# Kernel optimization log

Measured on AMD Instinct MI355X. Metric: run time of the kernel, lower is better.

The kernel has to match this reference:

```python
import jax, jax.numpy as jnp
import numpy as np

K = 1024  # init kwarg k


def setup_inputs() -> dict:
    key = jax.random.key(0)
    k1, k2 = jax.random.split(key)
    B, N, F = 8, 50000, 256
    node_embs = jax.random.normal(k1, (B, N, F), dtype=jnp.float32)
    mask = jnp.zeros((B, N), dtype=jnp.float32)  # additive mask (0 = keep)
    stdv = 1.0 / np.sqrt(F)
    scorer = jax.random.uniform(k2, (F, 1), dtype=jnp.float32, minval=-stdv, maxval=stdv)
    return {"node_embs": node_embs, "mask": mask, "scorer": scorer}


def reference(node_embs, mask, scorer):
    # scores: [B, N] = node_embs @ scorer / ||scorer||, plus additive mask
    scores = jnp.einsum('bnf,f->bn', node_embs, scorer[:, 0]) / jnp.linalg.norm(scorer)
    scores = scores + mask
    # top-k over node dim
    vals, topk_idx = jax.lax.top_k(scores, K)  # [B, K]
    # gather selected node embeddings and scale by tanh of their scores
    gathered = jnp.take_along_axis(node_embs, topk_idx[:, :, None], axis=1)  # [B, K, F]
    gate = jnp.tanh(jnp.take_along_axis(scores, topk_idx, axis=1))  # [B, K]
    out = gathered * gate[:, :, None]
    return out.transpose(0, 2, 1)  # [B, F, K]
```

## Files before the change

kernel.cpp:

```cpp
#include <hip/hip_runtime.h>
#include <math.h>

#define BB 8
#define NN 50000
#define FF 256
#define KK 1024
#define CHUNK 400
#define NCHUNK 125
#define NIT (CHUNK / 16)
#define CAPA 4096
#define RBLK 16

__device__ __forceinline__ unsigned long long key64(double x) {
    unsigned long long u = (unsigned long long)__double_as_longlong(x);
    u ^= (u & 0x8000000000000000ull) ? 0xFFFFFFFFFFFFFFFFull : 0x8000000000000000ull;
    return u;
}
__device__ __forceinline__ double key_to_double(unsigned long long k) {
    unsigned long long u = (k & 0x8000000000000000ull) ? (k ^ 0x8000000000000000ull) : ~k;
    return __longlong_as_double((long long)u);
}

__global__ __launch_bounds__(1024) void zero_kernel(unsigned int* __restrict__ p, int n) {
    int i = blockIdx.x * 1024 + threadIdx.x;
    if (i < n) p[i] = 0u;
}

__global__ __launch_bounds__(256) void score_kernel(const float* __restrict__ emb,
                                                    const float* __restrict__ mask,
                                                    const float* __restrict__ scorer,
                                                    double* __restrict__ scores,
                                                    unsigned int* __restrict__ ghist) {
    const int b    = blockIdx.x / NCHUNK;
    const int c    = blockIdx.x % NCHUNK;
    const int n0   = c * CHUNK;
    const int lane = threadIdx.x & 63;
    const int wave = threadIdx.x >> 6;
    const int s    = lane & 15;
    const int g    = lane >> 4;
    const int r0   = wave * 4 + g;

    __shared__ unsigned int h[2048];
    __shared__ float smask[CHUNK];
    for (int i = threadIdx.x; i < 2048; i += 256) h[i] = 0u;
    for (int i = threadIdx.x; i < CHUNK; i += 256) smask[i] = mask[b * NN + n0 + i];
    __syncthreads();

    double scd[16];
    {
        float4 f0 = ((const float4*)scorer)[s];
        float4 f1 = ((const float4*)scorer)[s + 16];
        float4 f2 = ((const float4*)scorer)[s + 32];
        float4 f3 = ((const float4*)scorer)[s + 48];
        scd[0]  = f0.x; scd[1]  = f0.y; scd[2]  = f0.z; scd[3]  = f0.w;
        scd[4]  = f1.x; scd[5]  = f1.y; scd[6]  = f1.z; scd[7]  = f1.w;
        scd[8]  = f2.x; scd[9]  = f2.y; scd[10] = f2.z; scd[11] = f2.w;
        scd[12] = f3.x; scd[13] = f3.y; scd[14] = f3.z; scd[15] = f3.w;
    }
    double n2 = 0.0;
    #pragma unroll
    for (int e = 0; e < 16; ++e) n2 += scd[e] * scd[e];
    #pragma unroll
    for (int off = 8; off; off >>= 1) n2 += __shfl_xor(n2, off, 64);
    const double inv_norm = 1.0 / sqrt(n2);

    const float* base  = emb + ((long)b * NN + n0) * FF;
    double*      sbase = scores + (long)b * NN + n0;

    auto step = [&](int it, const float4* vv) {
        double d = 0.0;
        #pragma unroll
        for (int i2 = 0; i2 < 4; ++i2) {
            d += (double)vv[i2].x * scd[4 * i2 + 0] + (double)vv[i2].y * scd[4 * i2 + 1] +
                 (double)vv[i2].z * scd[4 * i2 + 2] + (double)vv[i2].w * scd[4 * i2 + 3];
        }
        #pragma unroll
        for (int off = 8; off; off >>= 1) d += __shfl_xor(d, off, 64);
        if (s == 0) {
            const int row = it * 16 + r0;
            double sv = d * inv_norm + (double)smask[row];
            sbase[row] = sv;
            atomicAdd(&h[(unsigned)(key64(sv) >> 53)], 1u);
        }
    };

    const float* rp = base + r0 * FF;
    float4 v[4], w[4];
    #pragma unroll
    for (int i = 0; i < 4; ++i) v[i] = ((const float4*)rp)[s + 16 * i];

    for (int it = 0; it < NIT - 1; ++it) {
        rp += 16 * FF;
        #pragma unroll
        for (int i = 0; i < 4; ++i) w[i] = ((const float4*)rp)[s + 16 * i];
        step(it, v);
        #pragma unroll
        for (int i = 0; i < 4; ++i) v[i] = w[i];
    }
    step(NIT - 1, v);

    __syncthreads();
    unsigned int* gh = ghist + b * 2048;
    for (int i = threadIdx.x; i < 2048; i += 256) {
        unsigned int vv = h[i];
        if (vv) atomicAdd(&gh[i], vv);
    }
}

__global__ __launch_bounds__(1024) void candidates_kernel(const double* __restrict__ scores,
                                                          const unsigned int* __restrict__ ghist,
                                                          unsigned long long* __restrict__ ckey,
                                                          int* __restrict__ cidx,
                                                          unsigned int* __restrict__ ccnt) {
    const int b   = blockIdx.x;
    const int tid = threadIdx.x;
    const double* sc = scores + (long)b * NN;

    __shared__ unsigned int h[2048];
    __shared__ unsigned long long keyA[CAPA];
    __shared__ int idxA[CAPA];
    __shared__ int bin1_s, need2_s, bin2_s;
    __shared__ unsigned int cnt;

    const int i0 = tid, i1 = tid + 1024;

    h[i0] = ghist[b * 2048 + i0];
    h[i1] = ghist[b * 2048 + i1];
    if (tid == 0) cnt = 0u;
    __syncthreads();

    for (int off = 1; off < 2048; off <<= 1) {
        unsigned a0 = (i0 + off < 2048) ? h[i0 + off] : 0u;
        unsigned a1 = (i1 + off < 2048) ? h[i1 + off] : 0u;
        __syncthreads();
        h[i0] += a0; h[i1] += a1;
        __syncthreads();
    }
    if (h[i0] >= (unsigned)KK && (i0 == 2047 || h[i0 + 1] < (unsigned)KK)) {
        bin1_s = i0; need2_s = KK - (int)((i0 == 2047) ? 0u : h[i0 + 1]);
    }
    if (h[i1] >= (unsigned)KK && (i1 == 2047 || h[i1 + 1] < (unsigned)KK)) {
        bin1_s = i1; need2_s = KK - (int)((i1 == 2047) ? 0u : h[i1 + 1]);
    }
    __syncthreads();
    const unsigned long long bin1 = (unsigned long long)bin1_s;
    const unsigned need2 = (unsigned)need2_s;

    h[i0] = 0u; h[i1] = 0u;
    __syncthreads();
    for (int i = tid; i < NN / 2; i += 1024) {
        double2 v = ((const double2*)sc)[i];
        unsigned long long k0 = key64(v.x), k1 = key64(v.y);
        if ((k0 >> 53) == bin1) atomicAdd(&h[(unsigned)((k0 >> 42) & 2047ull)], 1u);
        if ((k1 >> 53) == bin1) atomicAdd(&h[(unsigned)((k1 >> 42) & 2047ull)], 1u);
    }
    __syncthreads();

    for (int off = 1; off < 2048; off <<= 1) {
        unsigned a0 = (i0 + off < 2048) ? h[i0 + off] : 0u;
        unsigned a1 = (i1 + off < 2048) ? h[i1 + off] : 0u;
        __syncthreads();
        h[i0] += a0; h[i1] += a1;
        __syncthreads();
    }
    if (h[i0] >= need2 && (i0 == 2047 || h[i0 + 1] < need2)) bin2_s = i0;
    if (h[i1] >= need2 && (i1 == 2047 || h[i1 + 1] < need2)) bin2_s = i1;
    __syncthreads();
    const unsigned long long pfx = (bin1 << 11) | (unsigned long long)bin2_s;

    for (int i = tid; i < NN / 2; i += 1024) {
        double2 v = ((const double2*)sc)[i];
        unsigned long long k0 = key64(v.x), k1 = key64(v.y);
        if ((k0 >> 42) >= pfx) {
            unsigned p = atomicAdd(&cnt, 1u);
            if (p < (unsigned)CAPA) { keyA[p] = k0; idxA[p] = 2 * i; }
        }
        if ((k1 >> 42) >= pfx) {
            unsigned p = atomicAdd(&cnt, 1u);
            if (p < (unsigned)CAPA) { keyA[p] = k1; idxA[p] = 2 * i + 1; }
        }
    }
    __syncthreads();
    const int M = (int)(cnt < (unsigned)CAPA ? cnt : (unsigned)CAPA);

    if (tid == 0) ccnt[b] = (unsigned)M;
    for (int i = tid; i < M; i += 1024) {
        ckey[b * CAPA + i] = keyA[i];
        cidx[b * CAPA + i] = idxA[i];
    }
}

__global__ __launch_bounds__(256) void rank_kernel(const unsigned long long* __restrict__ ckey,
                                                   const int* __restrict__ cidx,
                                                   const unsigned int* __restrict__ ccnt,
                                                   int* __restrict__ topk_idx,
                                                   float* __restrict__ gate) {
    const int b  = blockIdx.x >> 4;
    const int sl = blockIdx.x & (RBLK - 1);
    const int M  = (int)ccnt[b];
    const int r0 = sl * 256;
    if (r0 >= M) return;

    __shared__ unsigned long long k_s[CAPA];
    __shared__ int i_s[CAPA];

    const unsigned long long* kb = ckey + b * CAPA;
    const int* ib = cidx + b * CAPA;
    for (int i = threadIdx.x; i < M; i += 256) { k_s[i] = kb[i]; i_s[i] = ib[i]; }
    __syncthreads();

    const int r = r0 + threadIdx.x;
    if (r < M) {
        const unsigned long long kr = k_s[r];
        const int ir = i_s[r];
        int rank = 0;
        for (int j = 0; j < M; ++j) {
            const unsigned long long kj = k_s[j];
            rank += (kj > kr) || (kj == kr && i_s[j] < ir);
        }
        if (rank < KK) {
            topk_idx[b * KK + rank] = ir;
            gate[b * KK + rank]     = tanhf((float)key_to_double(kr));
        }
    }
}

__global__ __launch_bounds__(256) void gather_kernel(const float* __restrict__ emb,
                                                     const int* __restrict__ topk_idx,
                                                     const float* __restrict__ gate,
                                                     float* __restrict__ out) {
    const int b  = blockIdx.x >> 5;
    const int kt = blockIdx.x & 31;
    const int k0 = kt * 32;
    const int tid = threadIdx.x;

    __shared__ float tile[32][FF + 4];
    __shared__ int   s_idx[32];
    __shared__ float s_gate[32];

    if (tid < 32) {
        s_idx[tid]  = topk_idx[b * KK + k0 + tid];
        s_gate[tid] = gate[b * KK + k0 + tid];
    }
    __syncthreads();

    const int g = tid >> 6, lane = tid & 63;
    #pragma unroll
    for (int i = 0; i < 8; i++) {
        int kl = i * 4 + g;
        int row = s_idx[kl];
        float gt = s_gate[kl];
        float4 v = ((const float4*)(emb + ((long)b * NN + row) * FF))[lane];
        float* t = &tile[kl][lane * 4];
        t[0] = v.x * gt; t[1] = v.y * gt; t[2] = v.z * gt; t[3] = v.w * gt;
    }
    __syncthreads();

    const long outbase = ((long)b * FF) * KK + k0;
    #pragma unroll
    for (int c = 0; c < 32; c++) {
        int linear = c * 256 + tid;
        int f = linear >> 5;
        int k = linear & 31;
        out[outbase + (long)f * KK + k] = tile[k][f];
    }
}

extern "C" void kernel_launch(void* const* d_in, const int* in_sizes, int n_in,
                              void* d_out, int out_size, void* d_ws, size_t ws_size,
                              hipStream_t stream) {
    const float* emb    = (const float*)d_in[0];
    const float* mask   = (const float*)d_in[1];
    const float* scorer = (const float*)d_in[2];
    float* out = (float*)d_out;

    char* wsb = (char*)d_ws;
    double*             scores  = (double*)wsb;
    unsigned int*       ghist   = (unsigned int*)(wsb + sizeof(double) * BB * NN);
    int*                topkidx = (int*)((char*)ghist + sizeof(unsigned int) * BB * 2048);
    float*              gatep   = (float*)((char*)topkidx + sizeof(int) * BB * KK);
    unsigned long long* ckey    = (unsigned long long*)((char*)gatep + sizeof(float) * BB * KK);
    int*                cidx    = (int*)((char*)ckey + sizeof(unsigned long long) * BB * CAPA);
    unsigned int*       ccnt    = (unsigned int*)((char*)cidx + sizeof(int) * BB * CAPA);

    zero_kernel<<<16, 1024, 0, stream>>>(ghist, BB * 2048);
    score_kernel<<<BB * NCHUNK, 256, 0, stream>>>(emb, mask, scorer, scores, ghist);
    candidates_kernel<<<BB, 1024, 0, stream>>>(scores, ghist, ckey, cidx, ccnt);
    rank_kernel<<<BB * RBLK, 256, 0, stream>>>(ckey, cidx, ccnt, topkidx, gatep);
    gather_kernel<<<BB * 32, 256, 0, stream>>>(emb, topkidx, gatep, out);
}
```

Measured before the change: 650.4 us.

## Split per-batch candidate selection into multi-block histogram, scan and collect kernels

The single 8-block candidates kernel is split into four kernels. Two small scan kernels find the radix bins, and the two passes over the scores (second-level histogram and candidate collection) now run across 32 blocks per batch using global atomics. The aim is to spread the serial pass over 50k scores per batch across many CUs instead of 8. The cost is extra launches, global-memory atomic contention, and a nondeterministic candidate order.

```diff
diff --git a/kernel.cpp b/kernel.cpp
--- a/kernel.cpp
+++ b/kernel.cpp
@@ -10,6 +10,7 @@
 #define NIT (CHUNK / 16)
 #define CAPA 4096
 #define RBLK 16
+#define SB   32
 
 __device__ __forceinline__ unsigned long long key64(double x) {
     unsigned long long u = (unsigned long long)__double_as_longlong(x);
@@ -107,28 +108,14 @@
     }
 }
 
-__global__ __launch_bounds__(1024) void candidates_kernel(const double* __restrict__ scores,
-                                                          const unsigned int* __restrict__ ghist,
-                                                          unsigned long long* __restrict__ ckey,
-                                                          int* __restrict__ cidx,
-                                                          unsigned int* __restrict__ ccnt) {
-    const int b   = blockIdx.x;
-    const int tid = threadIdx.x;
-    const double* sc = scores + (long)b * NN;
-
+__global__ __launch_bounds__(1024) void scan1_kernel(const unsigned int* __restrict__ ghist,
+                                                     int* __restrict__ meta) {
+    const int b = blockIdx.x, tid = threadIdx.x;
     __shared__ unsigned int h[2048];
-    __shared__ unsigned long long keyA[CAPA];
-    __shared__ int idxA[CAPA];
-    __shared__ int bin1_s, need2_s, bin2_s;
-    __shared__ unsigned int cnt;
-
     const int i0 = tid, i1 = tid + 1024;
-
     h[i0] = ghist[b * 2048 + i0];
     h[i1] = ghist[b * 2048 + i1];
-    if (tid == 0) cnt = 0u;
-    __syncthreads();
-
+    __syncthreads();
     for (int off = 1; off < 2048; off <<= 1) {
         unsigned a0 = (i0 + off < 2048) ? h[i0 + off] : 0u;
         unsigned a1 = (i1 + off < 2048) ? h[i1 + off] : 0u;
@@ -137,25 +124,40 @@
         __syncthreads();
     }
     if (h[i0] >= (unsigned)KK && (i0 == 2047 || h[i0 + 1] < (unsigned)KK)) {
-        bin1_s = i0; need2_s = KK - (int)((i0 == 2047) ? 0u : h[i0 + 1]);
+        meta[b * 4 + 0] = i0;
+        meta[b * 4 + 1] = KK - (int)((i0 == 2047) ? 0u : h[i0 + 1]);
     }
     if (h[i1] >= (unsigned)KK && (i1 == 2047 || h[i1 + 1] < (unsigned)KK)) {
-        bin1_s = i1; need2_s = KK - (int)((i1 == 2047) ? 0u : h[i1 + 1]);
-    }
-    __syncthreads();
-    const unsigned long long bin1 = (unsigned long long)bin1_s;
-    const unsigned need2 = (unsigned)need2_s;
-
-    h[i0] = 0u; h[i1] = 0u;
-    __syncthreads();
-    for (int i = tid; i < NN / 2; i += 1024) {
+        meta[b * 4 + 0] = i1;
+        meta[b * 4 + 1] = KK - (int)((i1 == 2047) ? 0u : h[i1 + 1]);
+    }
+}
+
+__global__ __launch_bounds__(256) void hist2_kernel(const double* __restrict__ scores,
+                                                    const int* __restrict__ meta,
+                                                    unsigned int* __restrict__ ghist2) {
+    const int b = blockIdx.x / SB;
+    const int s = blockIdx.x % SB;
+    const unsigned long long bin1 = (unsigned long long)meta[b * 4 + 0];
+    const double* sc = scores + (long)b * NN;
+    unsigned int* h2 = ghist2 + b * 2048;
+    for (int i = s * 256 + threadIdx.x; i < NN / 2; i += SB * 256) {
         double2 v = ((const double2*)sc)[i];
         unsigned long long k0 = key64(v.x), k1 = key64(v.y);
-        if ((k0 >> 53) == bin1) atomicAdd(&h[(unsigned)((k0 >> 42) & 2047ull)], 1u);
-        if ((k1 >> 53) == bin1) atomicAdd(&h[(unsigned)((k1 >> 42) & 2047ull)], 1u);
-    }
-    __syncthreads();
-
+        if ((k0 >> 53) == bin1) atomicAdd(&h2[(unsigned)((k0 >> 42) & 2047ull)], 1u);
+        if ((k1 >> 53) == bin1) atomicAdd(&h2[(unsigned)((k1 >> 42) & 2047ull)], 1u);
+    }
+}
+
+__global__ __launch_bounds__(1024) void scan2_kernel(const unsigned int* __restrict__ ghist2,
+                                                     int* __restrict__ meta) {
+    const int b = blockIdx.x, tid = threadIdx.x;
+    const unsigned need2 = (unsigned)meta[b * 4 + 1];
+    __shared__ unsigned int h[2048];
+    const int i0 = tid, i1 = tid + 1024;
+    h[i0] = ghist2[b * 2048 + i0];
+    h[i1] = ghist2[b * 2048 + i1];
+    __syncthreads();
     for (int off = 1; off < 2048; off <<= 1) {
         unsigned a0 = (i0 + off < 2048) ? h[i0 + off] : 0u;
         unsigned a1 = (i1 + off < 2048) ? h[i1 + off] : 0u;
@@ -163,30 +165,31 @@
         h[i0] += a0; h[i1] += a1;
         __syncthreads();
     }
-    if (h[i0] >= need2 && (i0 == 2047 || h[i0 + 1] < need2)) bin2_s = i0;
-    if (h[i1] >= need2 && (i1 == 2047 || h[i1 + 1] < need2)) bin2_s = i1;
-    __syncthreads();
-    const unsigned long long pfx = (bin1 << 11) | (unsigned long long)bin2_s;
-
-    for (int i = tid; i < NN / 2; i += 1024) {
+    if (h[i0] >= need2 && (i0 == 2047 || h[i0 + 1] < need2)) meta[b * 4 + 2] = i0;
+    if (h[i1] >= need2 && (i1 == 2047 || h[i1 + 1] < need2)) meta[b * 4 + 2] = i1;
+}
+
+__global__ __launch_bounds__(256) void collect_kernel(const double* __restrict__ scores,
+                                                      const int* __restrict__ meta,
+                                                      unsigned long long* __restrict__ ckey,
+                                                      int* __restrict__ cidx,
+                                                      unsigned int* __restrict__ ccnt) {
+    const int b = blockIdx.x / SB;
+    const int s = blockIdx.x % SB;
+    const unsigned long long pfx =
+        ((unsigned long long)meta[b * 4 + 0] << 11) | (unsigned long long)meta[b * 4 + 2];
+    const double* sc = scores + (long)b * NN;
+    for (int i = s * 256 + threadIdx.x; i < NN / 2; i += SB * 256) {
         double2 v = ((const double2*)sc)[i];
         unsigned long long k0 = key64(v.x), k1 = key64(v.y);
         if ((k0 >> 42) >= pfx) {
-            unsigned p = atomicAdd(&cnt, 1u);
-            if (p < (unsigned)CAPA) { keyA[p] = k0; idxA[p] = 2 * i; }
+            unsigned p = atomicAdd(&ccnt[b], 1u);
+            if (p < (unsigned)CAPA) { ckey[b * CAPA + p] = k0; cidx[b * CAPA + p] = 2 * i; }
         }
         if ((k1 >> 42) >= pfx) {
-            unsigned p = atomicAdd(&cnt, 1u);
-            if (p < (unsigned)CAPA) { keyA[p] = k1; idxA[p] = 2 * i + 1; }
-        }
-    }
-    __syncthreads();
-    const int M = (int)(cnt < (unsigned)CAPA ? cnt : (unsigned)CAPA);
-
-    if (tid == 0) ccnt[b] = (unsigned)M;
-    for (int i = tid; i < M; i += 1024) {
-        ckey[b * CAPA + i] = keyA[i];
-        cidx[b * CAPA + i] = idxA[i];
+            unsigned p = atomicAdd(&ccnt[b], 1u);
+            if (p < (unsigned)CAPA) { ckey[b * CAPA + p] = k1; cidx[b * CAPA + p] = 2 * i + 1; }
+        }
     }
 }
 
@@ -197,7 +200,8 @@
                                                    float* __restrict__ gate) {
     const int b  = blockIdx.x >> 4;
     const int sl = blockIdx.x & (RBLK - 1);
-    const int M  = (int)ccnt[b];
+    const unsigned cm = ccnt[b];
+    const int M  = (int)(cm < (unsigned)CAPA ? cm : (unsigned)CAPA);
     const int r0 = sl * 256;
     if (r0 >= M) return;
 
@@ -277,15 +281,20 @@
     char* wsb = (char*)d_ws;
     double*             scores  = (double*)wsb;
     unsigned int*       ghist   = (unsigned int*)(wsb + sizeof(double) * BB * NN);
-    int*                topkidx = (int*)((char*)ghist + sizeof(unsigned int) * BB * 2048);
-    float*              gatep   = (float*)((char*)topkidx + sizeof(int) * BB * KK);
+    unsigned int*       ghist2  = ghist + BB * 2048;
+    unsigned int*       ccnt    = ghist2 + BB * 2048;
+    int*                meta    = (int*)(ccnt + BB);
+    int*                topkidx = meta + BB * 4;
+    float*              gatep   = (float*)(topkidx + BB * KK);
     unsigned long long* ckey    = (unsigned long long*)((char*)gatep + sizeof(float) * BB * KK);
     int*                cidx    = (int*)((char*)ckey + sizeof(unsigned long long) * BB * CAPA);
-    unsigned int*       ccnt    = (unsigned int*)((char*)cidx + sizeof(int) * BB * CAPA);
-
-    zero_kernel<<<16, 1024, 0, stream>>>(ghist, BB * 2048);
+
+    zero_kernel<<<(BB * 2048 * 2 + BB + 1023) / 1024, 1024, 0, stream>>>(ghist, BB * 2048 * 2 + BB);
     score_kernel<<<BB * NCHUNK, 256, 0, stream>>>(emb, mask, scorer, scores, ghist);
-    candidates_kernel<<<BB, 1024, 0, stream>>>(scores, ghist, ckey, cidx, ccnt);
+    scan1_kernel<<<BB, 1024, 0, stream>>>(ghist, meta);
+    hist2_kernel<<<BB * SB, 256, 0, stream>>>(scores, meta, ghist2);
+    scan2_kernel<<<BB, 1024, 0, stream>>>(ghist2, meta);
+    collect_kernel<<<BB * SB, 256, 0, stream>>>(scores, meta, ckey, cidx, ccnt);
     rank_kernel<<<BB * RBLK, 256, 0, stream>>>(ckey, cidx, ccnt, topkidx, gatep);
     gather_kernel<<<BB * 32, 256, 0, stream>>>(emb, topkidx, gatep, out);
 }
```

After: 685.3 us. 1.05x slower.
